# Kernel optimization log

Measured on AMD Instinct MI355X. Metric: run time of the kernel, lower is better.

## Reference

```python
import jax, jax.numpy as jnp
import numpy as np

WEIGHT_BIT = 8
ACT_BIT = 8
EPS = 1e-8

def ste_round(v):
    # straight-through estimator round (matches torch ste_round in QAT)
    return v + jax.lax.stop_gradient(jnp.round(v) - v)

def setup_inputs() -> dict:
    key = jax.random.key(0)
    k1, k2, k3, k4 = jax.random.split(key, 4)
    B, D_IN, D_OUT = 8192, 4096, 4096
    x = jax.random.normal(k1, (B, D_IN), dtype=jnp.float32)
    act_scaling_factor = jax.random.uniform(k2, (1,), dtype=jnp.float32, minval=0.01, maxval=0.05)
    W = jax.random.normal(k3, (D_OUT, D_IN), dtype=jnp.float32) * 0.02
    b = jax.random.normal(k4, (D_OUT,), dtype=jnp.float32) * 0.02
    return {"x": x, "act_scaling_factor": act_scaling_factor, "W": W, "b": b}

def reference(x, act_scaling_factor, W, b):
    n_w = 2 ** (WEIGHT_BIT - 1) - 1  # 127
    # ---- QuantLinear: symmetric per-channel weight quantization ----
    w_absmax = jnp.maximum(jnp.abs(W.min(axis=1)), jnp.abs(W.max(axis=1)))  # [out]
    fc_sf = jnp.maximum(w_absmax, EPS) / n_w  # weight scaling factor, [out]
    w_int = jnp.clip(ste_round(W / fc_sf[:, None]), -n_w - 1, n_w)
    bias_sf = fc_sf * act_scaling_factor  # [out] (act_sf is scalar-shaped [1])
    b_int = ste_round(b / bias_sf)
    x_int = x / act_scaling_factor
    out = (jnp.matmul(x_int, w_int.T) + b_int) * bias_sf  # [B, out]
    # ---- ReLU ----
    out = jax.nn.relu(out)
    # ---- QuantAct, asymmetric per-tensor requantization ----
    levels = 2 ** ACT_BIT - 1  # 255
    x_min = jnp.minimum(out.min(), 0.0)
    x_max = jnp.maximum(out.max(), 0.0)
    act_sf_new = jnp.maximum(x_max - x_min, EPS) / levels  # scalar
    zp = jnp.round(-x_min / act_sf_new)
    x_q = jnp.clip(ste_round(out / act_sf_new) + zp, 0.0, float(levels))
    x_out = (x_q - zp) * act_sf_new
    return (x_out, fc_sf, jnp.reshape(act_sf_new, (1,)))
```

## Files before the change

kernel.cpp:

```cpp
#include <hip/hip_runtime.h>
#include <hip/hip_bf16.h>
#include <stdint.h>

#define B_DIM 8192
#define IN_DIM 4096
#define OUT_DIM 4096
#define NT (IN_DIM / 64)

typedef __attribute__((ext_vector_type(8))) short s16x8;
typedef __attribute__((ext_vector_type(4))) float f32x4;

__device__ __forceinline__ unsigned short f2bf_rn(float f) {
    unsigned int u = __float_as_uint(f);
    u = (u + 0x7FFFu + ((u >> 16) & 1u)) >> 16;
    return (unsigned short)u;
}

__device__ __forceinline__ void async16(unsigned short* l, const unsigned short* g) {
    __builtin_amdgcn_global_load_lds(
        (const __attribute__((address_space(1))) void*)g,
        (__attribute__((address_space(3))) void*)l, 16, 0, 0);
}

__global__ __launch_bounds__(256) void prep(
    const float* __restrict__ W, const float* __restrict__ b,
    const float* __restrict__ act_sf, const float* __restrict__ x,
    unsigned short* __restrict__ wq, unsigned short* __restrict__ xq,
    float* __restrict__ fc_sf_out, float* __restrict__ bb,
    float* __restrict__ gmax)
{
    __shared__ float red[4];
    int t = threadIdx.x;
    if (blockIdx.x < OUT_DIM) {
        int o = blockIdx.x;
        const float4* Wr = (const float4*)(W + (size_t)o * IN_DIM);
        float4 v[4];
        float amax = 0.f;
#pragma unroll
        for (int j = 0; j < 4; ++j) {
            v[j] = Wr[t + j * 256];
            amax = fmaxf(amax, fmaxf(fmaxf(fabsf(v[j].x), fabsf(v[j].y)),
                                     fmaxf(fabsf(v[j].z), fabsf(v[j].w))));
        }
#pragma unroll
        for (int off = 32; off > 0; off >>= 1)
            amax = fmaxf(amax, __shfl_down(amax, off, 64));
        if ((t & 63) == 0) red[t >> 6] = amax;
        __syncthreads();
        float wmax = fmaxf(fmaxf(red[0], red[1]), fmaxf(red[2], red[3]));
        float sf = fmaxf(wmax, 1e-8f) / 127.0f;

        unsigned short* wr = wq + (size_t)o * IN_DIM;
#pragma unroll
        for (int j = 0; j < 4; ++j) {
            ushort4 q;
            q.x = f2bf_rn(fminf(fmaxf(rintf(v[j].x / sf), -128.f), 127.f));
            q.y = f2bf_rn(fminf(fmaxf(rintf(v[j].y / sf), -128.f), 127.f));
            q.z = f2bf_rn(fminf(fmaxf(rintf(v[j].z / sf), -128.f), 127.f));
            q.w = f2bf_rn(fminf(fmaxf(rintf(v[j].w / sf), -128.f), 127.f));
            ((ushort4*)wr)[t + j * 256] = q;
        }
        if (t == 0) {
            fc_sf_out[o] = sf;
            float bsf = sf * act_sf[0];
            float bi = rintf(b[o] / bsf);
            bb[o] = bi * bsf;
            if (o == 0) gmax[0] = 0.f;
        }
    } else {
        size_t i = ((size_t)(blockIdx.x - OUT_DIM) * 256 + t) * 8;
#pragma unroll
        for (int j = 0; j < 2; ++j) {
            float4 v = *(const float4*)(x + i + j * 4);
            ushort4 q;
            q.x = f2bf_rn(v.x); q.y = f2bf_rn(v.y);
            q.z = f2bf_rn(v.z); q.w = f2bf_rn(v.w);
            *(ushort4*)(xq + i + j * 4) = q;
        }
    }
}

template <bool CB16>
__global__ __launch_bounds__(512) void gemm_bt(
    const unsigned short* __restrict__ A, const unsigned short* __restrict__ Bw,
    const float* __restrict__ fc_sf, const float* __restrict__ bb,
    void* __restrict__ Cout, float* __restrict__ gmax)
{
    __shared__ __align__(16) unsigned char smem[131072];
    unsigned short* lds = (unsigned short*)smem;
    float* stage = (float*)smem;
    float* redm  = (float*)(smem + 131040);

    int t = threadIdx.x;
    int bid = ((blockIdx.x & 7) << 6) | (blockIdx.x >> 3);
    int bm = bid >> 4, bn = bid & 15;
    int m0 = bm << 8, n0 = bn << 8;

    int w = t >> 6, lane = t & 63;
    int wm = w & 1, wn = w >> 1;
    int quad = lane >> 4, l16 = lane & 15;
    int swz = l16 & 7;

    int co0 = (quad ^ swz) << 3;
    int co1 = ((quad + 4) ^ swz) << 3;
    int aOff = ((wm << 4) + l16) << 6;
    int bOff = 32768 + (((wn << 4) + l16) << 6);

    int r0 = t >> 3;
    int cs = ((t & 7) ^ (r0 & 7)) << 3;
    const unsigned short* gA = A + (size_t)(m0 + r0) * IN_DIM + cs;
    const unsigned short* gB = Bw + (size_t)(n0 + r0) * IN_DIM + cs;
    unsigned short* ldsA = lds + t * 8;
    unsigned short* ldsB = lds + 32768 + t * 8;

#define STA(u, hf) { int uu_ = (u) < NT ? (u) : ((u) - 2 < NT ? (u) - 2 : (u) - 4); \
    const unsigned short* s_ = gA + (size_t)((hf) * 128) * IN_DIM + uu_ * 64;       \
    unsigned short* d_ = ldsA + ((uu_ & 1) << 14) + ((hf) << 13);                   \
    async16(d_, s_); async16(d_ + 4096, s_ + (size_t)64 * IN_DIM); }
#define STB(u, hf) { int uu_ = (u) < NT ? (u) : ((u) - 2 < NT ? (u) - 2 : (u) - 4); \
    const unsigned short* s_ = gB + (size_t)((hf) * 128) * IN_DIM + uu_ * 64;       \
    unsigned short* d_ = ldsB + ((uu_ & 1) << 14) + ((hf) << 13);                   \
    async16(d_, s_); async16(d_ + 4096, s_ + (size_t)64 * IN_DIM); }

#define RD_A(dst, base) _Pragma("unroll") \
    for (int mi_ = 0; mi_ < 4; ++mi_) { \
        dst[mi_][0] = *(const s16x8*)((base) + mi_ * 2048 + co0); \
        dst[mi_][1] = *(const s16x8*)((base) + mi_ * 2048 + co1); }
#define RD_B(dst, base) _Pragma("unroll") \
    for (int nj_ = 0; nj_ < 2; ++nj_) { \
        dst[nj_][0] = *(const s16x8*)((base) + nj_ * 4096 + co0); \
        dst[nj_][1] = *(const s16x8*)((base) + nj_ * 4096 + co1); }

#define QUAD(MB, NB, AF, BF) _Pragma("unroll") \
    for (int mi_ = 0; mi_ < 4; ++mi_) { _Pragma("unroll") \
        for (int nj_ = 0; nj_ < 2; ++nj_) { \
            acc[(MB)+mi_][(NB)+nj_] = __builtin_amdgcn_mfma_f32_16x16x32_bf16( \
                AF[mi_][0], BF[nj_][0], acc[(MB)+mi_][(NB)+nj_], 0, 0, 0); \
            acc[(MB)+mi_][(NB)+nj_] = __builtin_amdgcn_mfma_f32_16x16x32_bf16( \
                AF[mi_][1], BF[nj_][1], acc[(MB)+mi_][(NB)+nj_], 0, 0, 0); } }

#define PHASE(RD, NCNT, ST, MM) \
    RD; \
    asm volatile("s_waitcnt lgkmcnt(" #NCNT ")" ::: "memory"); \
    __builtin_amdgcn_sched_barrier(0); \
    asm volatile("s_waitcnt vmcnt(10)" ::: "memory"); \
    __builtin_amdgcn_s_barrier(); \
    ST; \
    __builtin_amdgcn_s_setprio(1); \
    MM; \
    __builtin_amdgcn_s_setprio(0);

    f32x4 acc[8][4];
#pragma unroll
    for (int mi = 0; mi < 8; ++mi)
#pragma unroll
        for (int nj = 0; nj < 4; ++nj)
            acc[mi][nj] = (f32x4){0.f, 0.f, 0.f, 0.f};

    s16x8 a0[4][2], a1[4][2], b0[2][2], b1[2][2];

    STA(0, 0); STB(0, 0); STB(0, 1); STA(0, 1); STA(1, 0); STB(1, 0); STB(1, 1);
    asm volatile("s_waitcnt vmcnt(12)" ::: "memory");
    __builtin_amdgcn_s_barrier();
    RD_A(a0, lds + aOff);
    asm volatile("s_waitcnt lgkmcnt(8)" ::: "memory");
    __builtin_amdgcn_sched_barrier(0);
    asm volatile("s_waitcnt vmcnt(10)" ::: "memory");
    __builtin_amdgcn_s_barrier();
    STA(1, 1);
    RD_B(b0, lds + bOff);
    asm volatile("s_waitcnt lgkmcnt(4)" ::: "memory");
    __builtin_amdgcn_sched_barrier(0);
    asm volatile("s_waitcnt vmcnt(10)" ::: "memory");
    __builtin_amdgcn_s_barrier();
    STA(2, 0);

    for (int T = 0; T < NT; T += 2) {
        const unsigned short* laT  = lds + ((T & 1) << 14) + aOff;
        const unsigned short* lbT  = lds + ((T & 1) << 14) + bOff;
        const unsigned short* laT1 = lds + (((T + 1) & 1) << 14) + aOff;
        const unsigned short* lbT1 = lds + (((T + 1) & 1) << 14) + bOff;

        PHASE( RD_B(b1, lbT + 8192),  4, STB(T + 2, 0), QUAD(0, 0, a0, b0) );
        PHASE( RD_A(a1, laT + 8192),  8, STB(T + 2, 1), QUAD(0, 2, a0, b1) );
        PHASE( RD_A(a0, laT1),        8, STA(T + 2, 1), QUAD(4, 0, a1, b0) );
        PHASE( RD_B(b0, lbT1),        4, STA(T + 3, 0), QUAD(4, 2, a1, b1) );
        PHASE( RD_B(b1, lbT1 + 8192), 4, STB(T + 3, 0), QUAD(0, 0, a0, b0) );
        PHASE( RD_A(a1, laT1 + 8192), 8, STB(T + 3, 1), QUAD(0, 2, a0, b1) );
        PHASE( RD_A(a0, laT),         8, STA(T + 3, 1), QUAD(4, 0, a1, b0) );
        PHASE( RD_B(b0, lbT),         4, STA(T + 4, 0), QUAD(4, 2, a1, b1) );
    }

    asm volatile("s_waitcnt vmcnt(0) lgkmcnt(0)" ::: "memory");
    __syncthreads();

    float sc[4], bv[4];
#pragma unroll
    for (int nj = 0; nj < 4; ++nj) {
        int col = n0 + (((nj << 2) + wn) << 4) + l16;
        sc[nj] = fc_sf[col];
        bv[nj] = bb[col];
    }
    float tmax = 0.f;
#pragma unroll
    for (int mi = 0; mi < 8; ++mi)
#pragma unroll
        for (int nj = 0; nj < 4; ++nj)
#pragma unroll
            for (int r = 0; r < 4; ++r) {
                float vv = fmaxf(acc[mi][nj][r] * sc[nj] + bv[nj], 0.f);
                acc[mi][nj][r] = vv;
                tmax = fmaxf(tmax, vv);
            }
#pragma unroll
    for (int off = 32; off > 0; off >>= 1)
        tmax = fmaxf(tmax, __shfl_down(tmax, off, 64));
    if (lane == 0) redm[w] = tmax;

#pragma unroll
    for (int ph = 0; ph < 4; ++ph) {
        __syncthreads();
#pragma unroll
        for (int ml = 0; ml < 2; ++ml) {
            int lrow = (((ml << 1) + wm) << 4) + (quad << 2);
#pragma unroll
            for (int nj = 0; nj < 4; ++nj) {
                int col = (((nj << 2) + wn) << 4) + l16;
#pragma unroll
                for (int r = 0; r < 4; ++r)
                    stage[(lrow + r) * 260 + col] = acc[ph * 2 + ml][nj][r];
            }
        }
        __syncthreads();
        int row = t >> 3, ch = t & 7;
        const float* src = stage + row * 260 + ch * 32;
        size_t gbase = (size_t)(m0 + ph * 64 + row) * OUT_DIM + n0 + ch * 32;
        if (CB16) {
            unsigned short* dst = (unsigned short*)Cout + gbase;
#pragma unroll
            for (int j = 0; j < 4; ++j) {
                float4 v0 = *(const float4*)(src + j * 8);
                float4 v1 = *(const float4*)(src + j * 8 + 4);
                s16x8 q;
                q[0] = (short)f2bf_rn(v0.x); q[1] = (short)f2bf_rn(v0.y);
                q[2] = (short)f2bf_rn(v0.z); q[3] = (short)f2bf_rn(v0.w);
                q[4] = (short)f2bf_rn(v1.x); q[5] = (short)f2bf_rn(v1.y);
                q[6] = (short)f2bf_rn(v1.z); q[7] = (short)f2bf_rn(v1.w);
                *(s16x8*)(dst + j * 8) = q;
            }
        } else {
            float* dst = (float*)Cout + gbase;
#pragma unroll
            for (int j = 0; j < 8; ++j)
                *(float4*)(dst + j * 4) = *(const float4*)(src + j * 4);
        }
    }
    if (t == 0) {
        float bmax = redm[0];
#pragma unroll
        for (int i = 1; i < 8; ++i) bmax = fmaxf(bmax, redm[i]);
        atomicMax((int*)gmax, __float_as_int(bmax));
    }
#undef STA
#undef STB
#undef RD_A
#undef RD_B
#undef QUAD
#undef PHASE
}

template <bool CB16>
__global__ __launch_bounds__(256) void requant(const void* __restrict__ Cin,
    float* __restrict__ out, const float* __restrict__ gmax,
    float* __restrict__ sf_out)
{
    float sf = fmaxf(gmax[0], 1e-8f) / 255.0f;
    size_t i = ((size_t)blockIdx.x * 256 + threadIdx.x) * 16;
    if (CB16) {
        const unsigned short* cq = (const unsigned short*)Cin + i;
#pragma unroll
        for (int j = 0; j < 4; ++j) {
            ushort4 q = *(const ushort4*)(cq + j * 4);
            float4 v;
            v.x = __uint_as_float((unsigned)q.x << 16);
            v.y = __uint_as_float((unsigned)q.y << 16);
            v.z = __uint_as_float((unsigned)q.z << 16);
            v.w = __uint_as_float((unsigned)q.w << 16);
            v.x = fminf(rintf(v.x / sf), 255.f) * sf;
            v.y = fminf(rintf(v.y / sf), 255.f) * sf;
            v.z = fminf(rintf(v.z / sf), 255.f) * sf;
            v.w = fminf(rintf(v.w / sf), 255.f) * sf;
            *(float4*)(out + i + j * 4) = v;
        }
    } else {
        float* C = out;
#pragma unroll
        for (int j = 0; j < 4; ++j) {
            float4 v = *(const float4*)(C + i + j * 4);
            v.x = fminf(rintf(v.x / sf), 255.f) * sf;
            v.y = fminf(rintf(v.y / sf), 255.f) * sf;
            v.z = fminf(rintf(v.z / sf), 255.f) * sf;
            v.w = fminf(rintf(v.w / sf), 255.f) * sf;
            *(float4*)(C + i + j * 4) = v;
        }
    }
    if (i == 0) sf_out[0] = sf;
}

extern "C" void kernel_launch(void* const* d_in, const int* in_sizes, int n_in,
                              void* d_out, int out_size, void* d_ws, size_t ws_size,
                              hipStream_t stream)
{
    const float* x      = (const float*)d_in[0];
    const float* act_sf = (const float*)d_in[1];
    const float* W      = (const float*)d_in[2];
    const float* b      = (const float*)d_in[3];

    float* out        = (float*)d_out;
    float* fc_sf_out  = out + (size_t)B_DIM * OUT_DIM;
    float* act_sf_out = fc_sf_out + OUT_DIM;

    char* ws = (char*)d_ws;
    float* bb   = (float*)ws;
    float* gmax = (float*)(ws + 16384);
    unsigned short* xq = (unsigned short*)(ws + 32768);
    unsigned short* wq = xq + (size_t)B_DIM * IN_DIM;
    unsigned short* cq = wq + (size_t)OUT_DIM * IN_DIM;

    size_t need = 32768 + ((size_t)B_DIM * IN_DIM + (size_t)OUT_DIM * IN_DIM
                           + (size_t)B_DIM * OUT_DIM) * 2;

    prep<<<OUT_DIM + (B_DIM * IN_DIM) / 2048, 256, 0, stream>>>(
        W, b, act_sf, x, wq, xq, fc_sf_out, bb, gmax);

    int gemm_grid = (B_DIM / 256) * (OUT_DIM / 256);
    int rq_grid = (B_DIM * OUT_DIM) / 4096;
    if (ws_size >= need) {
        gemm_bt<true><<<gemm_grid, 512, 0, stream>>>(
            xq, wq, fc_sf_out, bb, (void*)cq, gmax);
        requant<true><<<rq_grid, 256, 0, stream>>>(
            (const void*)cq, out, gmax, act_sf_out);
    } else {
        gemm_bt<false><<<gemm_grid, 512, 0, stream>>>(
            xq, wq, fc_sf_out, bb, (void*)out, gmax);
        requant<false><<<rq_grid, 256, 0, stream>>>(
            (const void*)out, out, gmax, act_sf_out);
    }
}
```

Baseline: 527.3 us.

## Switch GEMM inner loop from 16x16x32 to 32x32x16 bf16 MFMA

Replaces the 16x16x32 MFMA tiling with 32x32x16 bf16 MFMA instructions. The LDS fragment read offsets, accumulator layout (f32x16) and epilogue staging indices are remapped to match. Larger MFMA tiles raise operand reuse per LDS read and cut the instruction count. The cost is a different register layout and possibly new LDS bank access patterns.

```diff
diff --git a/kernel.cpp b/kernel.cpp
--- a/kernel.cpp
+++ b/kernel.cpp
@@ -9,6 +9,7 @@
 
 typedef __attribute__((ext_vector_type(8))) short s16x8;
 typedef __attribute__((ext_vector_type(4))) float f32x4;
+typedef __attribute__((ext_vector_type(16))) float f32x16;
 
 __device__ __forceinline__ unsigned short f2bf_rn(float f) {
     unsigned int u = __float_as_uint(f);
@@ -98,13 +99,14 @@
 
     int w = t >> 6, lane = t & 63;
     int wm = w & 1, wn = w >> 1;
-    int quad = lane >> 4, l16 = lane & 15;
-    int swz = l16 & 7;
-
-    int co0 = (quad ^ swz) << 3;
-    int co1 = ((quad + 4) ^ swz) << 3;
-    int aOff = ((wm << 4) + l16) << 6;
-    int bOff = 32768 + (((wn << 4) + l16) << 6);
+    int l31 = lane & 31, lhi = lane >> 5, l7 = lane & 7;
+
+    int co32[4];
+#pragma unroll
+    for (int ks = 0; ks < 4; ++ks)
+        co32[ks] = (((2 * ks + lhi) ^ l7) << 3);
+    int aOff = ((wm << 5) + l31) << 6;
+    int bOff = 32768 + (((wn << 5) + l31) << 6);
 
     int r0 = t >> 3;
     int cs = ((t & 7) ^ (r0 & 7)) << 3;
@@ -123,21 +125,18 @@
     async16(d_, s_); async16(d_ + 4096, s_ + (size_t)64 * IN_DIM); }
 
 #define RD_A(dst, base) _Pragma("unroll") \
-    for (int mi_ = 0; mi_ < 4; ++mi_) { \
-        dst[mi_][0] = *(const s16x8*)((base) + mi_ * 2048 + co0); \
-        dst[mi_][1] = *(const s16x8*)((base) + mi_ * 2048 + co1); }
+    for (int mh_ = 0; mh_ < 2; ++mh_) { _Pragma("unroll") \
+        for (int ks_ = 0; ks_ < 4; ++ks_) \
+            dst[mh_][ks_] = *(const s16x8*)((base) + mh_ * 4096 + co32[ks_]); }
 #define RD_B(dst, base) _Pragma("unroll") \
-    for (int nj_ = 0; nj_ < 2; ++nj_) { \
-        dst[nj_][0] = *(const s16x8*)((base) + nj_ * 4096 + co0); \
-        dst[nj_][1] = *(const s16x8*)((base) + nj_ * 4096 + co1); }
-
-#define QUAD(MB, NB, AF, BF) _Pragma("unroll") \
-    for (int mi_ = 0; mi_ < 4; ++mi_) { _Pragma("unroll") \
-        for (int nj_ = 0; nj_ < 2; ++nj_) { \
-            acc[(MB)+mi_][(NB)+nj_] = __builtin_amdgcn_mfma_f32_16x16x32_bf16( \
-                AF[mi_][0], BF[nj_][0], acc[(MB)+mi_][(NB)+nj_], 0, 0, 0); \
-            acc[(MB)+mi_][(NB)+nj_] = __builtin_amdgcn_mfma_f32_16x16x32_bf16( \
-                AF[mi_][1], BF[nj_][1], acc[(MB)+mi_][(NB)+nj_], 0, 0, 0); } }
+    for (int ks_ = 0; ks_ < 4; ++ks_) \
+        dst[ks_] = *(const s16x8*)((base) + co32[ks_]);
+
+#define QUAD(X, Y, AF, BF) _Pragma("unroll") \
+    for (int mh_ = 0; mh_ < 2; ++mh_) { _Pragma("unroll") \
+        for (int ks_ = 0; ks_ < 4; ++ks_) \
+            acc[2 * (X) + mh_][Y] = __builtin_amdgcn_mfma_f32_32x32x16_bf16( \
+                AF[mh_][ks_], BF[ks_], acc[2 * (X) + mh_][Y], 0, 0, 0); }
 
 #define PHASE(RD, NCNT, ST, MM) \
     RD; \
@@ -150,14 +149,16 @@
     MM; \
     __builtin_amdgcn_s_setprio(0);
 
-    f32x4 acc[8][4];
-#pragma unroll
-    for (int mi = 0; mi < 8; ++mi)
-#pragma unroll
-        for (int nj = 0; nj < 4; ++nj)
-            acc[mi][nj] = (f32x4){0.f, 0.f, 0.f, 0.f};
-
-    s16x8 a0[4][2], a1[4][2], b0[2][2], b1[2][2];
+    f32x16 acc[4][2];
+#pragma unroll
+    for (int m = 0; m < 4; ++m)
+#pragma unroll
+        for (int y = 0; y < 2; ++y)
+#pragma unroll
+            for (int r = 0; r < 16; ++r)
+                acc[m][y][r] = 0.f;
+
+    s16x8 a0[2][4], a1[2][4], b0[4], b1[4];
 
     STA(0, 0); STB(0, 0); STB(0, 1); STA(0, 1); STA(1, 0); STB(1, 0); STB(1, 1);
     asm volatile("s_waitcnt vmcnt(12)" ::: "memory");
@@ -182,34 +183,34 @@
         const unsigned short* lbT1 = lds + (((T + 1) & 1) << 14) + bOff;
 
         PHASE( RD_B(b1, lbT + 8192),  4, STB(T + 2, 0), QUAD(0, 0, a0, b0) );
-        PHASE( RD_A(a1, laT + 8192),  8, STB(T + 2, 1), QUAD(0, 2, a0, b1) );
-        PHASE( RD_A(a0, laT1),        8, STA(T + 2, 1), QUAD(4, 0, a1, b0) );
-        PHASE( RD_B(b0, lbT1),        4, STA(T + 3, 0), QUAD(4, 2, a1, b1) );
+        PHASE( RD_A(a1, laT + 8192),  8, STB(T + 2, 1), QUAD(0, 1, a0, b1) );
+        PHASE( RD_A(a0, laT1),        8, STA(T + 2, 1), QUAD(1, 0, a1, b0) );
+        PHASE( RD_B(b0, lbT1),        4, STA(T + 3, 0), QUAD(1, 1, a1, b1) );
         PHASE( RD_B(b1, lbT1 + 8192), 4, STB(T + 3, 0), QUAD(0, 0, a0, b0) );
-        PHASE( RD_A(a1, laT1 + 8192), 8, STB(T + 3, 1), QUAD(0, 2, a0, b1) );
-        PHASE( RD_A(a0, laT),         8, STA(T + 3, 1), QUAD(4, 0, a1, b0) );
-        PHASE( RD_B(b0, lbT),         4, STA(T + 4, 0), QUAD(4, 2, a1, b1) );
+        PHASE( RD_A(a1, laT1 + 8192), 8, STB(T + 3, 1), QUAD(0, 1, a0, b1) );
+        PHASE( RD_A(a0, laT),         8, STA(T + 3, 1), QUAD(1, 0, a1, b0) );
+        PHASE( RD_B(b0, lbT),         4, STA(T + 4, 0), QUAD(1, 1, a1, b1) );
     }
 
     asm volatile("s_waitcnt vmcnt(0) lgkmcnt(0)" ::: "memory");
     __syncthreads();
 
-    float sc[4], bv[4];
-#pragma unroll
-    for (int nj = 0; nj < 4; ++nj) {
-        int col = n0 + (((nj << 2) + wn) << 4) + l16;
-        sc[nj] = fc_sf[col];
-        bv[nj] = bb[col];
+    float sc[2], bv[2];
+#pragma unroll
+    for (int y = 0; y < 2; ++y) {
+        int col = n0 + (((y << 2) + wn) << 5) + l31;
+        sc[y] = fc_sf[col];
+        bv[y] = bb[col];
     }
     float tmax = 0.f;
 #pragma unroll
-    for (int mi = 0; mi < 8; ++mi)
-#pragma unroll
-        for (int nj = 0; nj < 4; ++nj)
-#pragma unroll
-            for (int r = 0; r < 4; ++r) {
-                float vv = fmaxf(acc[mi][nj][r] * sc[nj] + bv[nj], 0.f);
-                acc[mi][nj][r] = vv;
+    for (int m = 0; m < 4; ++m)
+#pragma unroll
+        for (int y = 0; y < 2; ++y)
+#pragma unroll
+            for (int r = 0; r < 16; ++r) {
+                float vv = fmaxf(acc[m][y][r] * sc[y] + bv[y], 0.f);
+                acc[m][y][r] = vv;
                 tmax = fmaxf(tmax, vv);
             }
 #pragma unroll
@@ -221,14 +222,12 @@
     for (int ph = 0; ph < 4; ++ph) {
         __syncthreads();
 #pragma unroll
-        for (int ml = 0; ml < 2; ++ml) {
-            int lrow = (((ml << 1) + wm) << 4) + (quad << 2);
-#pragma unroll
-            for (int nj = 0; nj < 4; ++nj) {
-                int col = (((nj << 2) + wn) << 4) + l16;
-#pragma unroll
-                for (int r = 0; r < 4; ++r)
-                    stage[(lrow + r) * 260 + col] = acc[ph * 2 + ml][nj][r];
+        for (int y = 0; y < 2; ++y) {
+            int col = (((y << 2) + wn) << 5) + l31;
+#pragma unroll
+            for (int r = 0; r < 16; ++r) {
+                int lrow = (wm << 5) + (r & 3) + ((r >> 2) << 3) + (lhi << 2);
+                stage[lrow * 260 + col] = acc[ph][y][r];
             }
         }
         __syncthreads();
```

Result: slower. 552.2 us (+4.7%).
